# Optimization experiments

Measured on AMD Instinct MI355X. Metric: run time of the kernel, lower is better.

Reference implementation:

```python
import jax, jax.numpy as jnp
import numpy as np


def setup_inputs() -> dict:
    key = jax.random.key(0)
    k1, k2 = jax.random.split(key)
    B, S, D = 8, 4096, 1024
    E, P = 8, 4
    x = jax.random.normal(k1, (B, S, D), dtype=jnp.float32)
    phi_kernel = jax.random.normal(k2, (D, E * P), dtype=jnp.float32) * (1.0 / np.sqrt(D))
    phi_bias = jnp.zeros((E * P,), dtype=jnp.float32)
    return {"x": x, "phi_kernel": phi_kernel, "phi_bias": phi_bias,
            "num_experts": E, "num_slots": P}


def reference(x, phi_kernel, phi_bias, num_experts, num_slots):
    B, S, D = x.shape
    E, P = num_experts, num_slots
    # phi logits: [B,S,E,P]
    phi_logits = (jnp.einsum('bsd,dk->bsk', x, phi_kernel) + phi_bias).reshape(B, S, E, P)
    # softmax over the sequence axis (each slot is a convex combo of tokens)
    phi_weights = jax.nn.softmax(phi_logits, axis=1)
    # soft slots: weighted sum over tokens -> [B,E,P,D] (fused, no [B,S,E,P,D] blowup)
    soft_slots = jnp.einsum('bsd,bsep->bepd', x, phi_weights)
    expert_inputs = soft_slots.reshape(B, E, P * D)
    expert_weights = jnp.full((B, S, E), 1.0 / E, dtype=x.dtype)
    expert_indices = jnp.broadcast_to(jnp.arange(E, dtype=jnp.int32)[None, None, :], (B, S, E))
    return (expert_weights, expert_indices, phi_weights, soft_slots, expert_inputs)
```

## Files before the change

kernel.cpp:

```cpp
#include <hip/hip_runtime.h>
#include <hip/hip_bf16.h>

#define B 8
#define S 4096
#define DD 1024
#define KK 32

typedef __attribute__((ext_vector_type(8))) short bf16x8;
typedef __attribute__((ext_vector_type(16))) float f32x16;

static __device__ __forceinline__ unsigned short f2bf(float f) {
    unsigned int u = __builtin_bit_cast(unsigned int, f);
    u += 0x7FFFu + ((u >> 16) & 1u);
    return (unsigned short)(u >> 16);
}

static __device__ __forceinline__ unsigned int pack2bf(float lo, float hi) {
    return (unsigned int)f2bf(lo) | ((unsigned int)f2bf(hi) << 16);
}

static __device__ __forceinline__ void gload_lds16(const void* g, void* l) {
    __builtin_amdgcn_global_load_lds(
        (const __attribute__((address_space(1))) unsigned int*)g,
        (__attribute__((address_space(3))) unsigned int*)l, 16, 0, 0);
}

__global__ __launch_bounds__(256) void k0_phit(const float* __restrict__ phi,
                                               unsigned short* __restrict__ phiT) {
    __shared__ float lt[32][33];
    const int d0 = blockIdx.x * 32;
    const int tid = threadIdx.x;
#pragma unroll
    for (int i = 0; i < 4; ++i) {
        int slot = tid + i * 256;
        int d = slot >> 5, k = slot & 31;
        lt[d][k] = phi[(size_t)(d0 + d) * KK + k];
    }
    __syncthreads();
    const int k = tid >> 3, c = tid & 7, d = c * 4;
    short4 pk;
    pk.x = (short)f2bf(lt[d + 0][k]);
    pk.y = (short)f2bf(lt[d + 1][k]);
    pk.z = (short)f2bf(lt[d + 2][k]);
    pk.w = (short)f2bf(lt[d + 3][k]);
    *(short4*)(phiT + (size_t)k * DD + d0 + d) = pk;
}

__global__ __launch_bounds__(256) void k1_logits(const float* __restrict__ x,
                                                 const unsigned short* __restrict__ phiT,
                                                 const float* __restrict__ bias,
                                                 float* __restrict__ lp,
                                                 float* __restrict__ pmax,
                                                 float* __restrict__ psum) {
    __shared__ __align__(16) char sm[65536];

    const int bid = blockIdx.x;
    const int st = bid & 63;
    const int b  = bid >> 6;
    const int tid = threadIdx.x;
    const int wv = __builtin_amdgcn_readfirstlane(tid >> 6);
    const int lane = tid & 63;
    const int l31 = lane & 31;
    const int half = lane >> 5;
    const int r0 = (wv >> 1) * 32;
    const int h  = wv & 1;

    {
        const uint4* pg = (const uint4*)phiT;
#pragma unroll
        for (int i = 0; i < 16; ++i) {
            int slot = tid + i * 256;
            int k = slot >> 7, blk = slot & 127;
            uint4 v = pg[(size_t)k * 128 + blk];
            *(uint4*)(sm + (size_t)k * 2048 + ((blk ^ (k & 7)) << 4)) = v;
        }
    }

    f32x16 acc;
    {
        float bv = (h == 0) ? bias[l31] : 0.f;
#pragma unroll
        for (int r = 0; r < 16; ++r) acc[r] = bv;
    }
    __syncthreads();

    const float* xg = x + ((size_t)(b * S + st * 64 + r0 + l31)) * DD
                        + h * 512 + half * 8;
    const int kx = l31 & 7;
    const char* brow = sm + (size_t)l31 * 2048;

#pragma unroll 8
    for (int ch = 0; ch < 32; ++ch) {
        float4 a0 = *(const float4*)(xg + ch * 16);
        float4 a1 = *(const float4*)(xg + ch * 16 + 4);
        unsigned int p0 = pack2bf(a0.x, a0.y);
        unsigned int p1 = pack2bf(a0.z, a0.w);
        unsigned int p2 = pack2bf(a1.x, a1.y);
        unsigned int p3 = pack2bf(a1.z, a1.w);
        uint4 pv = make_uint4(p0, p1, p2, p3);
        bf16x8 af = __builtin_bit_cast(bf16x8, pv);
        int blk = h * 64 + ch * 2 + half;
        bf16x8 bfv = *(const bf16x8*)(brow + ((blk ^ kx) << 4));
        acc = __builtin_amdgcn_mfma_f32_32x32x16_bf16(af, bfv, acc, 0, 0, 0);
    }

    __syncthreads();
    float* lt = (float*)sm;
    if (h == 0) {
#pragma unroll
        for (int r = 0; r < 16; ++r) {
            int row = (r & 3) + 8 * (r >> 2) + 4 * half;
            lt[(size_t)l31 * 65 + r0 + row] = acc[r];
        }
    }
    __syncthreads();
    if (h == 1) {
#pragma unroll
        for (int r = 0; r < 16; ++r) {
            int row = (r & 3) + 8 * (r >> 2) + 4 * half;
            lt[(size_t)l31 * 65 + r0 + row] += acc[r];
        }
    }
    __syncthreads();

    float* o = lp + ((size_t)b * KK) * S + st * 64;
#pragma unroll
    for (int i = 0; i < 2; ++i) {
        int slot = tid + i * 256;
        int k = slot >> 4, s4 = slot & 15;
        float4 v;
        v.x = lt[k * 65 + s4 * 4 + 0];
        v.y = lt[k * 65 + s4 * 4 + 1];
        v.z = lt[k * 65 + s4 * 4 + 2];
        v.w = lt[k * 65 + s4 * 4 + 3];
        *(float4*)(o + (size_t)k * S + s4 * 4) = v;
    }

    const int pk = tid >> 3, pj = tid & 7;
    const float* lr = lt + (size_t)pk * 65 + pj * 8;
    float m = lr[0];
#pragma unroll
    for (int i = 1; i < 8; ++i) m = fmaxf(m, lr[i]);
#pragma unroll
    for (int off = 4; off >= 1; off >>= 1) m = fmaxf(m, __shfl_xor(m, off, 64));
    float l = 0.f;
#pragma unroll
    for (int i = 0; i < 8; ++i) l += __expf(lr[i] - m);
#pragma unroll
    for (int off = 4; off >= 1; off >>= 1) l += __shfl_xor(l, off, 64);
    if (pj == 0) {
        pmax[((size_t)b * KK + pk) * 64 + st] = m;
        psum[((size_t)b * KK + pk) * 64 + st] = l;
    }
}

__global__ __launch_bounds__(256) void k2c_norm(const float* __restrict__ lp,
                                                const float* __restrict__ pmax,
                                                const float* __restrict__ psum,
                                                unsigned short* __restrict__ wbT,
                                                float* __restrict__ pw_out) {
    __shared__ float tile[128][33];
    __shared__ float sM[32], sLinv[32];
    const int b  = blockIdx.x >> 5;
    const int sc = blockIdx.x & 31;
    const int s0 = sc * 128;
    const int tid = threadIdx.x;

    {
        const int k = tid >> 3, pj = tid & 7;
        float M = -1e30f, L = 0.f;
#pragma unroll
        for (int c = 0; c < 8; ++c) {
            int cc = pj * 8 + c;
            float mc = pmax[((size_t)b * KK + k) * 64 + cc];
            float lc = psum[((size_t)b * KK + k) * 64 + cc];
            float nM = fmaxf(M, mc);
            L = L * __expf(M - nM) + lc * __expf(mc - nM);
            M = nM;
        }
#pragma unroll
        for (int off = 4; off >= 1; off >>= 1) {
            float Mo = __shfl_xor(M, off, 64);
            float Lo = __shfl_xor(L, off, 64);
            float nM = fmaxf(M, Mo);
            L = L * __expf(M - nM) + Lo * __expf(Mo - nM);
            M = nM;
        }
        if (pj == 0) {
            sM[k] = M;
            sLinv[k] = 1.0f / L;
        }
    }
    __syncthreads();

    const int sL = tid & 127;
    const int kh = tid >> 7;
#pragma unroll
    for (int kk = 0; kk < 16; ++kk) {
        const int k = kk * 2 + kh;
        const size_t idx = ((size_t)b * KK + k) * S + s0 + sL;
        float v = lp[idx];
        float w = __expf(v - sM[k]) * sLinv[k];
        wbT[idx] = f2bf(w);
        tile[sL][k] = w;
    }
    __syncthreads();

    float* ob = pw_out + ((size_t)b * S + s0) * KK;
#pragma unroll
    for (int i = 0; i < 4; ++i) {
        const int idx4 = tid + i * 256;
        const int sl = idx4 >> 3, kq = idx4 & 7;
        float4 v4 = make_float4(tile[sl][kq * 4 + 0], tile[sl][kq * 4 + 1],
                                tile[sl][kq * 4 + 2], tile[sl][kq * 4 + 3]);
        ((float4*)ob)[idx4] = v4;
    }
}

__global__ __launch_bounds__(256) void k3_slots(const float* __restrict__ x,
                                                const unsigned short* __restrict__ wbT,
                                                float* __restrict__ part) {
    __shared__ __align__(16) char sm[2 * 32768 + 2 * 4096];

    const int bid = blockIdx.x;
    const int sc = bid & 7;
    const int dg = (bid >> 3) & 7;
    const int b  = bid >> 6;
    const int tid = threadIdx.x;
    const int wv = __builtin_amdgcn_readfirstlane(tid >> 6);
    const int lane = tid & 63;
    const int l31 = lane & 31;
    const int half = lane >> 5;

    const char* xsrc = (const char*)(x + ((size_t)(b * S + sc * 512 + wv * 16 + half)) * DD
                                       + dg * 128 + l31 * 4);
    const int wk = wv * 8 + (lane >> 3);
    const char* wsrc = (const char*)wbT + ((size_t)(b * KK + wk) * S + sc * 512) * 2
                                        + (((lane & 7) ^ (wk & 7)) << 4);

    char* const xb0 = sm;
    char* const wb0 = sm + 65536;

    auto stage = [&](int ch, int buf) {
        char* xb = xb0 + buf * 32768 + wv * (16 * 512);
        const char* xs = xsrc + (size_t)ch * (64 * DD * 4);
#pragma unroll
        for (int t = 0; t < 8; ++t)
            gload_lds16(xs + (size_t)t * (2 * DD * 4), xb + t * 1024);
        gload_lds16(wsrc + (size_t)ch * 128, wb0 + buf * 4096 + wv * 1024);
    };

    f32x16 acc;
#pragma unroll
    for (int r = 0; r < 16; ++r) acc[r] = 0.f;

    stage(0, 0);
    __syncthreads();

    const int col = wv * 32 + l31;
    const int kx = l31 & 7;

    for (int ch = 0; ch < 8; ++ch) {
        const int cur = ch & 1;
        if (ch < 7) stage(ch + 1, cur ^ 1);
        const float* xr = (const float*)(xb0 + cur * 32768);
        const char* wr = wb0 + cur * 4096 + (size_t)l31 * 128;
#pragma unroll
        for (int step = 0; step < 4; ++step) {
            bf16x8 af = *(const bf16x8*)(wr + (((step * 2 + half) ^ kx) << 4));
            const int sb = step * 16 + half * 8;
            unsigned int p0 = pack2bf(xr[(sb + 0) * 128 + col], xr[(sb + 1) * 128 + col]);
            unsigned int p1 = pack2bf(xr[(sb + 2) * 128 + col], xr[(sb + 3) * 128 + col]);
            unsigned int p2 = pack2bf(xr[(sb + 4) * 128 + col], xr[(sb + 5) * 128 + col]);
            unsigned int p3 = pack2bf(xr[(sb + 6) * 128 + col], xr[(sb + 7) * 128 + col]);
            uint4 pv = make_uint4(p0, p1, p2, p3);
            bf16x8 bfv = __builtin_bit_cast(bf16x8, pv);
            acc = __builtin_amdgcn_mfma_f32_32x32x16_bf16(af, bfv, acc, 0, 0, 0);
        }
        __syncthreads();
    }

    float* pp = part + (((size_t)sc * B + b) * KK) * DD + dg * 128 + col;
#pragma unroll
    for (int r = 0; r < 16; ++r) {
        int k = (r & 3) + 8 * (r >> 2) + 4 * half;
        pp[(size_t)k * DD] = acc[r];
    }
}

__global__ __launch_bounds__(256) void k4_finalize(const float* __restrict__ part,
                                                   float* __restrict__ out) {
    const int idx = blockIdx.x * 256 + threadIdx.x;
    const float4* p4 = (const float4*)part;

    float4 sv = p4[idx];
#pragma unroll
    for (int c = 1; c < 8; ++c) {
        float4 t = p4[(size_t)c * 65536 + idx];
        sv.x += t.x; sv.y += t.y; sv.z += t.z; sv.w += t.w;
    }

    ((float4*)(out + 1572864))[idx] = sv;
    ((float4*)(out + 1835008))[idx] = sv;
    ((float4*)out)[idx] = make_float4(0.125f, 0.125f, 0.125f, 0.125f);
    float base = (float)((idx * 4) & 7);
    ((float4*)(out + 262144))[idx] = make_float4(base, base + 1.f, base + 2.f, base + 3.f);
}

extern "C" void kernel_launch(void* const* d_in, const int* in_sizes, int n_in,
                              void* d_out, int out_size, void* d_ws, size_t ws_size,
                              hipStream_t stream) {
    const float* x    = (const float*)d_in[0];
    const float* phi  = (const float*)d_in[1];
    const float* bias = (const float*)d_in[2];
    float* out = (float*)d_out;

    float* ws = (float*)d_ws;
    float* lp   = ws;
    float* pmax = ws + 1048576;
    float* psum = ws + 1064960;
    unsigned short* wbT  = (unsigned short*)(ws + 1081344);
    unsigned short* phiT = (unsigned short*)(ws + 1605632);
    float* part = ws + 1622016;
    float* pw_out = out + 524288;

    k0_phit<<<dim3(32), dim3(256), 0, stream>>>(phi, phiT);
    k1_logits<<<dim3(512), dim3(256), 0, stream>>>(x, phiT, bias, lp, pmax, psum);
    k2c_norm<<<dim3(256), dim3(256), 0, stream>>>(lp, pmax, psum, wbT, pw_out);
    k3_slots<<<dim3(512), dim3(256), 0, stream>>>(x, wbT, part);
    k4_finalize<<<dim3(256), dim3(256), 0, stream>>>(part, out);
}
```

Measured before the change: 228.1 us.

## Load x and weights directly from global in slot kernel, drop LDS staging

```diff
diff --git a/kernel.cpp b/kernel.cpp
--- a/kernel.cpp
+++ b/kernel.cpp
@@ -17,12 +17,6 @@
 
 static __device__ __forceinline__ unsigned int pack2bf(float lo, float hi) {
     return (unsigned int)f2bf(lo) | ((unsigned int)f2bf(hi) << 16);
-}
-
-static __device__ __forceinline__ void gload_lds16(const void* g, void* l) {
-    __builtin_amdgcn_global_load_lds(
-        (const __attribute__((address_space(1))) unsigned int*)g,
-        (__attribute__((address_space(3))) unsigned int*)l, 16, 0, 0);
 }
 
 __global__ __launch_bounds__(256) void k0_phit(const float* __restrict__ phi,
@@ -217,11 +211,9 @@
     }
 }
 
-__global__ __launch_bounds__(256) void k3_slots(const float* __restrict__ x,
-                                                const unsigned short* __restrict__ wbT,
-                                                float* __restrict__ part) {
-    __shared__ __align__(16) char sm[2 * 32768 + 2 * 4096];
-
+__global__ __launch_bounds__(256, 4) void k3_slots(const float* __restrict__ x,
+                                                   const unsigned short* __restrict__ wbT,
+                                                   float* __restrict__ part) {
     const int bid = blockIdx.x;
     const int sc = bid & 7;
     const int dg = (bid >> 3) & 7;
@@ -231,53 +223,27 @@
     const int lane = tid & 63;
     const int l31 = lane & 31;
     const int half = lane >> 5;
-
-    const char* xsrc = (const char*)(x + ((size_t)(b * S + sc * 512 + wv * 16 + half)) * DD
-                                       + dg * 128 + l31 * 4);
-    const int wk = wv * 8 + (lane >> 3);
-    const char* wsrc = (const char*)wbT + ((size_t)(b * KK + wk) * S + sc * 512) * 2
-                                        + (((lane & 7) ^ (wk & 7)) << 4);
-
-    char* const xb0 = sm;
-    char* const wb0 = sm + 65536;
-
-    auto stage = [&](int ch, int buf) {
-        char* xb = xb0 + buf * 32768 + wv * (16 * 512);
-        const char* xs = xsrc + (size_t)ch * (64 * DD * 4);
-#pragma unroll
-        for (int t = 0; t < 8; ++t)
-            gload_lds16(xs + (size_t)t * (2 * DD * 4), xb + t * 1024);
-        gload_lds16(wsrc + (size_t)ch * 128, wb0 + buf * 4096 + wv * 1024);
-    };
+    const int col = wv * 32 + l31;
+
+    const float* xg = x + ((size_t)(b * S + sc * 512 + half * 8)) * DD + dg * 128 + col;
+    const unsigned short* wg = wbT + ((size_t)(b * KK + l31)) * S + sc * 512 + half * 8;
 
     f32x16 acc;
 #pragma unroll
     for (int r = 0; r < 16; ++r) acc[r] = 0.f;
 
-    stage(0, 0);
-    __syncthreads();
-
-    const int col = wv * 32 + l31;
-    const int kx = l31 & 7;
-
-    for (int ch = 0; ch < 8; ++ch) {
-        const int cur = ch & 1;
-        if (ch < 7) stage(ch + 1, cur ^ 1);
-        const float* xr = (const float*)(xb0 + cur * 32768);
-        const char* wr = wb0 + cur * 4096 + (size_t)l31 * 128;
-#pragma unroll
-        for (int step = 0; step < 4; ++step) {
-            bf16x8 af = *(const bf16x8*)(wr + (((step * 2 + half) ^ kx) << 4));
-            const int sb = step * 16 + half * 8;
-            unsigned int p0 = pack2bf(xr[(sb + 0) * 128 + col], xr[(sb + 1) * 128 + col]);
-            unsigned int p1 = pack2bf(xr[(sb + 2) * 128 + col], xr[(sb + 3) * 128 + col]);
-            unsigned int p2 = pack2bf(xr[(sb + 4) * 128 + col], xr[(sb + 5) * 128 + col]);
-            unsigned int p3 = pack2bf(xr[(sb + 6) * 128 + col], xr[(sb + 7) * 128 + col]);
-            uint4 pv = make_uint4(p0, p1, p2, p3);
-            bf16x8 bfv = __builtin_bit_cast(bf16x8, pv);
-            acc = __builtin_amdgcn_mfma_f32_32x32x16_bf16(af, bfv, acc, 0, 0, 0);
-        }
-        __syncthreads();
+#pragma unroll 4
+    for (int t = 0; t < 32; ++t) {
+        const int sb = t * 16;
+        bf16x8 af = *(const bf16x8*)(wg + sb);
+        const float* xp = xg + (size_t)sb * DD;
+        unsigned int p0 = pack2bf(xp[0],               xp[(size_t)1 * DD]);
+        unsigned int p1 = pack2bf(xp[(size_t)2 * DD],  xp[(size_t)3 * DD]);
+        unsigned int p2 = pack2bf(xp[(size_t)4 * DD],  xp[(size_t)5 * DD]);
+        unsigned int p3 = pack2bf(xp[(size_t)6 * DD],  xp[(size_t)7 * DD]);
+        uint4 pv = make_uint4(p0, p1, p2, p3);
+        bf16x8 bfv = __builtin_bit_cast(bf16x8, pv);
+        acc = __builtin_amdgcn_mfma_f32_32x32x16_bf16(af, bfv, acc, 0, 0, 0);
     }
 
     float* pp = part + (((size_t)sc * B + b) * KK) * DD + dg * 128 + col;
```

Measured after the change: 229.7 us. Within noise of the previous version (+0.7%).
